# Kernel optimization log

Hardware: AMD Instinct MI355X
Metric: run time of the kernel (lower is better)

Reference implementation:

```python
import jax, jax.numpy as jnp
import numpy as np

N_NODES = 100000
N_EDGES = 3200000
IN_SIZE = 256
HID_SIZE = 256
OUT_SIZE = 64


def setup_inputs() -> dict:
    key = jax.random.key(0)
    ks = jax.random.split(key, 8)
    X = jax.random.normal(ks[0], (N_NODES, IN_SIZE), dtype=jnp.float32)
    edge_vals = jax.random.uniform(ks[1], (N_EDGES,), dtype=jnp.float32)
    # xavier-uniform-ish init for weights
    lim1 = float(np.sqrt(6.0 / (IN_SIZE + HID_SIZE)))
    W1 = jax.random.uniform(ks[2], (IN_SIZE, HID_SIZE), minval=-lim1, maxval=lim1, dtype=jnp.float32)
    b1 = jnp.zeros((HID_SIZE,), dtype=jnp.float32)
    lim2 = float(np.sqrt(6.0 / (HID_SIZE + OUT_SIZE)))
    W2 = jax.random.uniform(ks[3], (HID_SIZE, OUT_SIZE), minval=-lim2, maxval=lim2, dtype=jnp.float32)
    b2 = jnp.zeros((OUT_SIZE,), dtype=jnp.float32)
    row = jnp.sort(jax.random.randint(ks[4], (N_EDGES,), 0, N_NODES, dtype=jnp.int32))
    col = jax.random.randint(ks[5], (N_EDGES,), 0, N_NODES, dtype=jnp.int32)
    return {"X": X, "edge_vals": edge_vals, "W1": W1, "b1": b1,
            "W2": W2, "b2": b2, "row": row, "col": col}


def reference(X, edge_vals, W1, b1, W2, b2, row, col):
    """2-layer GCN (eval mode, dropout = identity).

    A is a sparse NxN matrix in COO form: A[row[e], col[e]] = edge_vals[e].
    Layer: relu(A @ (X @ W1) + b1); output: A @ (h @ W2) + b2.
    """
    n = X.shape[0]

    def spmm(dense):  # (A @ dense): gather columns, scale, segment-sum over rows
        gathered = edge_vals[:, None] * dense[col]        # [E, F]
        return jax.ops.segment_sum(gathered, row, num_segments=n)

    h = spmm(X @ W1) + b1          # [N, HID]
    h = jax.nn.relu(h)
    out = spmm(h @ W2) + b2        # [N, OUT]
    return out
```

## Files before the change

### kernel.cpp

```cpp
#include <hip/hip_runtime.h>


constexpr int IN_SIZE = 256;
constexpr int HID = 256;
constexpr int OUTF = 64;

typedef __bf16 bf16x8 __attribute__((ext_vector_type(8)));
typedef float f32x4 __attribute__((ext_vector_type(4)));

__device__ __forceinline__ ushort f2b(float f) {
    uint u = __float_as_uint(f);
    uint r = (u + 0x7fffu + ((u >> 16) & 1u)) >> 16;
    return (ushort)r;
}
__device__ __forceinline__ float b2f(ushort h) {
    return __uint_as_float(((uint)h) << 16);
}

__global__ void build_rowptr(const int* __restrict__ row, int* __restrict__ rp,
                             int n, int E) {
    int i = blockIdx.x * blockDim.x + threadIdx.x;
    if (i > n) return;
    int lo = 0, hi = E;
    while (lo < hi) {
        int mid = (lo + hi) >> 1;
        if (row[mid] < i) lo = mid + 1; else hi = mid;
    }
    rp[i] = lo;
}

__global__ void transpose_cast(const float* __restrict__ in, ushort* __restrict__ out,
                               int K, int N) {
    int n = blockIdx.x;
    int k = threadIdx.x;
    if (k < K) out[(size_t)n * K + k] = f2b(in[(size_t)k * N + n]);
}

__global__ __launch_bounds__(256, 2)
void gemm1_cast_n256(const float* __restrict__ A, const ushort* __restrict__ Bt,
                     ushort* __restrict__ C, int M) {
    constexpr int K = 256;
    __shared__ ushort As[128 * 40];
    __shared__ ushort Bs[256 * 40];
    const int tid = threadIdx.x;
    const int wave = tid >> 6, lane = tid & 63;
    const int quad = lane >> 4, l = lane & 15;
    const int wr = wave >> 1, wc = wave & 1;
    const int m0 = blockIdx.x * 128;

    const int ar = tid >> 1;
    const int ah = (tid & 1) * 16;
    const size_t aoff = (size_t)min(m0 + ar, M - 1) * K + ah;
    const int bn = tid >> 2;
    const int bkp = (tid & 3) * 8;

    f32x4 acc[4][8] = {};

    for (int k0 = 0; k0 < K; k0 += 32) {
        float4 a0 = *(const float4*)(A + aoff + k0);
        float4 a1 = *(const float4*)(A + aoff + k0 + 4);
        float4 a2 = *(const float4*)(A + aoff + k0 + 8);
        float4 a3 = *(const float4*)(A + aoff + k0 + 12);
        uint4 bv[4];
#pragma unroll
        for (int j = 0; j < 4; ++j)
            bv[j] = *(const uint4*)(Bt + (size_t)(bn + 64 * j) * K + k0 + bkp);
        uint4 pa0, pa1;
        pa0.x = (uint)f2b(a0.x) | ((uint)f2b(a0.y) << 16);
        pa0.y = (uint)f2b(a0.z) | ((uint)f2b(a0.w) << 16);
        pa0.z = (uint)f2b(a1.x) | ((uint)f2b(a1.y) << 16);
        pa0.w = (uint)f2b(a1.z) | ((uint)f2b(a1.w) << 16);
        pa1.x = (uint)f2b(a2.x) | ((uint)f2b(a2.y) << 16);
        pa1.y = (uint)f2b(a2.z) | ((uint)f2b(a2.w) << 16);
        pa1.z = (uint)f2b(a3.x) | ((uint)f2b(a3.y) << 16);
        pa1.w = (uint)f2b(a3.z) | ((uint)f2b(a3.w) << 16);
        __syncthreads();
        *(uint4*)&As[ar * 40 + ah] = pa0;
        *(uint4*)&As[ar * 40 + ah + 8] = pa1;
#pragma unroll
        for (int j = 0; j < 4; ++j)
            *(uint4*)&Bs[(bn + 64 * j) * 40 + bkp] = bv[j];
        __syncthreads();

        bf16x8 af[4], bfr[8];
        const ushort* ab = &As[(wr * 64 + l) * 40 + quad * 8];
#pragma unroll
        for (int mt = 0; mt < 4; ++mt)
            af[mt] = *(const bf16x8*)(ab + mt * 16 * 40);
        const ushort* bb = &Bs[(wc * 128 + l) * 40 + quad * 8];
#pragma unroll
        for (int nt = 0; nt < 8; ++nt)
            bfr[nt] = *(const bf16x8*)(bb + nt * 16 * 40);
#pragma unroll
        for (int mt = 0; mt < 4; ++mt)
#pragma unroll
            for (int nt = 0; nt < 8; ++nt)
                acc[mt][nt] = __builtin_amdgcn_mfma_f32_16x16x32_bf16(
                    af[mt], bfr[nt], acc[mt][nt], 0, 0, 0);
    }

#pragma unroll
    for (int mt = 0; mt < 4; ++mt)
#pragma unroll
        for (int nt = 0; nt < 8; ++nt)
#pragma unroll
            for (int reg = 0; reg < 4; ++reg) {
                int r = m0 + wr * 64 + mt * 16 + quad * 4 + reg;
                int c = wc * 128 + nt * 16 + l;
                if (r < M) C[(size_t)r * 256 + c] = f2b(acc[mt][nt][reg]);
            }
}

__global__ __launch_bounds__(256, 4)
void gemm_bf16(const ushort* __restrict__ A, const ushort* __restrict__ Bt,
               ushort* __restrict__ C, int M, int N, int K) {
    __shared__ ushort As[128 * 40];
    __shared__ ushort Bs[64 * 40];
    const int tid = threadIdx.x;
    const int wave = tid >> 6, lane = tid & 63;
    const int quad = lane >> 4, l = lane & 15;
    const int wr = wave >> 1, wc = wave & 1;
    const int m0 = blockIdx.x * 128, n0 = blockIdx.y * 64;

    const int crow = tid >> 2;
    const int cpart = (tid & 3) * 8;
    const size_t aoff0 = (size_t)min(m0 + crow, M - 1) * K + cpart;
    const size_t aoff1 = (size_t)min(m0 + crow + 64, M - 1) * K + cpart;
    const size_t boff  = (size_t)(n0 + crow) * K + cpart;

    f32x4 acc[4][2] = {};

    for (int k0 = 0; k0 < K; k0 += 32) {
        uint4 a0 = *(const uint4*)(A + aoff0 + k0);
        uint4 a1 = *(const uint4*)(A + aoff1 + k0);
        uint4 b0 = *(const uint4*)(Bt + boff + k0);
        __syncthreads();
        *(uint4*)&As[crow * 40 + cpart] = a0;
        *(uint4*)&As[(crow + 64) * 40 + cpart] = a1;
        *(uint4*)&Bs[crow * 40 + cpart] = b0;
        __syncthreads();

        bf16x8 af[4], bfr[2];
        const ushort* ab = &As[(wr * 64 + l) * 40 + quad * 8];
#pragma unroll
        for (int mt = 0; mt < 4; ++mt)
            af[mt] = *(const bf16x8*)(ab + mt * 16 * 40);
        const ushort* bb = &Bs[(wc * 32 + l) * 40 + quad * 8];
#pragma unroll
        for (int nt = 0; nt < 2; ++nt)
            bfr[nt] = *(const bf16x8*)(bb + nt * 16 * 40);
#pragma unroll
        for (int mt = 0; mt < 4; ++mt)
#pragma unroll
            for (int nt = 0; nt < 2; ++nt)
                acc[mt][nt] = __builtin_amdgcn_mfma_f32_16x16x32_bf16(
                    af[mt], bfr[nt], acc[mt][nt], 0, 0, 0);
    }

#pragma unroll
    for (int mt = 0; mt < 4; ++mt)
#pragma unroll
        for (int nt = 0; nt < 2; ++nt)
#pragma unroll
            for (int reg = 0; reg < 4; ++reg) {
                int r = m0 + wr * 64 + mt * 16 + quad * 4 + reg;
                int c = n0 + wc * 32 + nt * 16 + l;
                if (r < M) C[(size_t)r * N + c] = f2b(acc[mt][nt][reg]);
            }
}

__global__ __launch_bounds__(256)
void quant_rows_256(const ushort* __restrict__ Sb, char* __restrict__ Q,
                    float* __restrict__ scale, int n) {
    const int wave = threadIdx.x >> 6;
    const int lane = threadIdx.x & 63;
    const int node = blockIdx.x * 4 + wave;
    if (node >= n) return;
    ushort4 x = *(const ushort4*)(Sb + (size_t)node * 256 + lane * 4);
    float f0 = b2f(x.x), f1 = b2f(x.y), f2 = b2f(x.z), f3 = b2f(x.w);
    float am = fmaxf(fmaxf(fabsf(f0), fabsf(f1)), fmaxf(fabsf(f2), fabsf(f3)));
#pragma unroll
    for (int s = 32; s >= 1; s >>= 1) am = fmaxf(am, __shfl_xor(am, s));
    float inv = am > 0.f ? 127.f / am : 0.f;
    int q0 = (int)rintf(f0 * inv), q1 = (int)rintf(f1 * inv);
    int q2 = (int)rintf(f2 * inv), q3 = (int)rintf(f3 * inv);
    uint qp = ((uint)q0 & 0xff) | (((uint)q1 & 0xff) << 8) |
              (((uint)q2 & 0xff) << 16) | (((uint)q3 & 0xff) << 24);
    *(uint*)(Q + (size_t)node * 256 + lane * 4) = qp;
    if (lane == 0) scale[node] = am * (1.f / 127.f);
}

__global__ __launch_bounds__(256)
void quant_rows_64(const ushort* __restrict__ Sb, char* __restrict__ Q,
                   float* __restrict__ scale, int n) {
    const int wave = threadIdx.x >> 6;
    const int lane = threadIdx.x & 63;
    const int node = blockIdx.x * 4 + wave;
    if (node >= n) return;
    float f = b2f(Sb[(size_t)node * 64 + lane]);
    float am = fabsf(f);
#pragma unroll
    for (int s = 32; s >= 1; s >>= 1) am = fmaxf(am, __shfl_xor(am, s));
    float inv = am > 0.f ? 127.f / am : 0.f;
    Q[(size_t)node * 64 + lane] = (char)(int)rintf(f * inv);
    if (lane == 0) scale[node] = am * (1.f / 127.f);
}

__global__ __launch_bounds__(256)
void spmm1_q(const char* __restrict__ Q, const float* __restrict__ s1,
             const float* __restrict__ vals, const int* __restrict__ col,
             const int* __restrict__ rp, const float* __restrict__ bias,
             ushort* __restrict__ H, int n) {
    const int wave = threadIdx.x >> 6;
    const int lane = threadIdx.x & 63;
    const int node = blockIdx.x * 4 + wave;
    if (node >= n) return;
    const int e0 = rp[node], e1 = rp[node + 1];
    float a0 = 0.f, a1 = 0.f, a2 = 0.f, a3 = 0.f;
    int e = e0;
    for (; e + 7 < e1; e += 8) {
#pragma unroll
        for (int u = 0; u < 8; ++u) {
            int c = col[e + u];
            float f = vals[e + u] * s1[c];
            char4 q = *(const char4*)(Q + (size_t)c * 256 + lane * 4);
            a0 += f * (float)q.x;
            a1 += f * (float)q.y;
            a2 += f * (float)q.z;
            a3 += f * (float)q.w;
        }
    }
    for (; e < e1; ++e) {
        int c = col[e];
        float f = vals[e] * s1[c];
        char4 q = *(const char4*)(Q + (size_t)c * 256 + lane * 4);
        a0 += f * (float)q.x;
        a1 += f * (float)q.y;
        a2 += f * (float)q.z;
        a3 += f * (float)q.w;
    }
    float4 b = *(const float4*)(bias + lane * 4);
    ushort4 r;
    r.x = f2b(fmaxf(a0 + b.x, 0.f));
    r.y = f2b(fmaxf(a1 + b.y, 0.f));
    r.z = f2b(fmaxf(a2 + b.z, 0.f));
    r.w = f2b(fmaxf(a3 + b.w, 0.f));
    *(ushort4*)(H + (size_t)node * 256 + lane * 4) = r;
}

__global__ __launch_bounds__(256)
void spmm2_q(const char* __restrict__ Q, const float* __restrict__ s2,
             const float* __restrict__ vals, const int* __restrict__ col,
             const int* __restrict__ rp, const float* __restrict__ bias,
             float* __restrict__ O, int n) {
    const int wave = threadIdx.x >> 6;
    const int lane = threadIdx.x & 63;
    const int node = blockIdx.x * 4 + wave;
    if (node >= n) return;
    const int e0 = rp[node], e1 = rp[node + 1];
    float acc = 0.f;
    int e = e0;
    for (; e + 7 < e1; e += 8) {
#pragma unroll
        for (int u = 0; u < 8; ++u) {
            int c = col[e + u];
            float f = vals[e + u] * s2[c];
            acc += f * (float)Q[(size_t)c * 64 + lane];
        }
    }
    for (; e < e1; ++e) {
        int c = col[e];
        acc += vals[e] * s2[c] * (float)Q[(size_t)c * 64 + lane];
    }
    O[(size_t)node * 64 + lane] = acc + bias[lane];
}

static inline size_t alignup(size_t x) { return (x + 255) & ~(size_t)255; }

extern "C" void kernel_launch(void* const* d_in, const int* in_sizes, int n_in,
                              void* d_out, int out_size, void* d_ws, size_t ws_size,
                              hipStream_t stream) {
    const float* X  = (const float*)d_in[0];
    const float* ev = (const float*)d_in[1];
    const float* W1 = (const float*)d_in[2];
    const float* b1 = (const float*)d_in[3];
    const float* W2 = (const float*)d_in[4];
    const float* b2 = (const float*)d_in[5];
    const int*  row = (const int*)d_in[6];
    const int*  col = (const int*)d_in[7];
    float* out = (float*)d_out;

    const int n = in_sizes[0] / IN_SIZE;
    const int E = in_sizes[1];

    char* p = (char*)d_ws;
    ushort* C1  = (ushort*)p; p += alignup((size_t)n * HID * 2);
    char*   Q1  = (char*)p;   p += alignup((size_t)n * HID);
    float*  s1  = (float*)p;  p += alignup((size_t)n * 4);
    ushort* H   = (ushort*)p; p += alignup((size_t)n * HID * 2);
    ushort* hw2 = (ushort*)p; p += alignup((size_t)n * OUTF * 2);
    char*   Q2  = (char*)p;   p += alignup((size_t)n * OUTF);
    float*  s2  = (float*)p;  p += alignup((size_t)n * 4);
    ushort* W1T = (ushort*)p; p += alignup((size_t)IN_SIZE * HID * 2);
    ushort* W2T = (ushort*)p; p += alignup((size_t)HID * OUTF * 2);
    int*    rp  = (int*)p;

    build_rowptr<<<(n + 1 + 255) / 256, 256, 0, stream>>>(row, rp, n, E);
    transpose_cast<<<dim3(HID, 1), 256, 0, stream>>>(W1, W1T, IN_SIZE, HID);
    transpose_cast<<<dim3(OUTF, 1), 256, 0, stream>>>(W2, W2T, HID, OUTF);

    gemm1_cast_n256<<<(n + 127) / 128, 256, 0, stream>>>(X, W1T, C1, n);

    quant_rows_256<<<(n + 3) / 4, 256, 0, stream>>>(C1, Q1, s1, n);

    spmm1_q<<<(n + 3) / 4, 256, 0, stream>>>(Q1, s1, ev, col, rp, b1, H, n);

    dim3 g2((n + 127) / 128, OUTF / 64);
    gemm_bf16<<<g2, 256, 0, stream>>>(H, W2T, hw2, n, OUTF, HID);

    quant_rows_64<<<(n + 3) / 4, 256, 0, stream>>>(hw2, Q2, s2, n);

    spmm2_q<<<(n + 3) / 4, 256, 0, stream>>>(Q2, s2, ev, col, rp, b2, out, n);
}
```

Before: 525.2 us.

## Precompute packed edge (col, scaled weight) arrays and shrink GEMM1 tile

Adds a prep_edges kernel that folds the per-node quantization scale into each edge value and packs it with the column index as an int2. Both SpMM kernels then read that array instead of col, vals and a random s[c] gather. This removes a dependent random load per edge at the cost of an extra pass over the edges writing and reading E*8 bytes per layer. GEMM1 moves to 64-row tiles with one wave per 64-column slice, and the C1/H buffers are aliased to cut workspace footprint.

```diff
diff --git a/kernel.cpp b/kernel.cpp
--- a/kernel.cpp
+++ b/kernel.cpp
@@ -36,65 +36,64 @@
     if (k < K) out[(size_t)n * K + k] = f2b(in[(size_t)k * N + n]);
 }
 
-__global__ __launch_bounds__(256, 2)
-void gemm1_cast_n256(const float* __restrict__ A, const ushort* __restrict__ Bt,
-                     ushort* __restrict__ C, int M) {
+__global__ void prep_edges(const float* __restrict__ vals, const int* __restrict__ col,
+                           const float* __restrict__ s, int2* __restrict__ ew, int E) {
+    int e = blockIdx.x * 256 + threadIdx.x;
+    if (e >= E) return;
+    int c = col[e];
+    float w = vals[e] * s[c];
+    ew[e] = make_int2(c, __float_as_int(w));
+}
+
+__global__ __launch_bounds__(256)
+void gemm1_cast(const float* __restrict__ A, const ushort* __restrict__ Bt,
+                ushort* __restrict__ C, int M) {
     constexpr int K = 256;
-    __shared__ ushort As[128 * 40];
+    __shared__ ushort As[64 * 40];
     __shared__ ushort Bs[256 * 40];
     const int tid = threadIdx.x;
     const int wave = tid >> 6, lane = tid & 63;
     const int quad = lane >> 4, l = lane & 15;
-    const int wr = wave >> 1, wc = wave & 1;
-    const int m0 = blockIdx.x * 128;
-
-    const int ar = tid >> 1;
-    const int ah = (tid & 1) * 16;
-    const size_t aoff = (size_t)min(m0 + ar, M - 1) * K + ah;
+    const int m0 = blockIdx.x * 64;
+
+    const int ar = tid >> 2;
+    const int ak = (tid & 3) * 8;
+    const size_t aoff = (size_t)min(m0 + ar, M - 1) * K + ak;
     const int bn = tid >> 2;
     const int bkp = (tid & 3) * 8;
 
-    f32x4 acc[4][8] = {};
+    f32x4 acc[4][4] = {};
 
     for (int k0 = 0; k0 < K; k0 += 32) {
         float4 a0 = *(const float4*)(A + aoff + k0);
         float4 a1 = *(const float4*)(A + aoff + k0 + 4);
-        float4 a2 = *(const float4*)(A + aoff + k0 + 8);
-        float4 a3 = *(const float4*)(A + aoff + k0 + 12);
         uint4 bv[4];
 #pragma unroll
         for (int j = 0; j < 4; ++j)
             bv[j] = *(const uint4*)(Bt + (size_t)(bn + 64 * j) * K + k0 + bkp);
-        uint4 pa0, pa1;
-        pa0.x = (uint)f2b(a0.x) | ((uint)f2b(a0.y) << 16);
-        pa0.y = (uint)f2b(a0.z) | ((uint)f2b(a0.w) << 16);
-        pa0.z = (uint)f2b(a1.x) | ((uint)f2b(a1.y) << 16);
-        pa0.w = (uint)f2b(a1.z) | ((uint)f2b(a1.w) << 16);
-        pa1.x = (uint)f2b(a2.x) | ((uint)f2b(a2.y) << 16);
-        pa1.y = (uint)f2b(a2.z) | ((uint)f2b(a2.w) << 16);
-        pa1.z = (uint)f2b(a3.x) | ((uint)f2b(a3.y) << 16);
-        pa1.w = (uint)f2b(a3.z) | ((uint)f2b(a3.w) << 16);
+        uint4 pa;
+        pa.x = (uint)f2b(a0.x) | ((uint)f2b(a0.y) << 16);
+        pa.y = (uint)f2b(a0.z) | ((uint)f2b(a0.w) << 16);
+        pa.z = (uint)f2b(a1.x) | ((uint)f2b(a1.y) << 16);
+        pa.w = (uint)f2b(a1.z) | ((uint)f2b(a1.w) << 16);
         __syncthreads();
-        *(uint4*)&As[ar * 40 + ah] = pa0;
-        *(uint4*)&As[ar * 40 + ah + 8] = pa1;
+        *(uint4*)&As[ar * 40 + ak] = pa;
 #pragma unroll
         for (int j = 0; j < 4; ++j)
             *(uint4*)&Bs[(bn + 64 * j) * 40 + bkp] = bv[j];
         __syncthreads();
 
-        bf16x8 af[4], bfr[8];
-        const ushort* ab = &As[(wr * 64 + l) * 40 + quad * 8];
+        bf16x8 af[4], bfr[4];
 #pragma unroll
         for (int mt = 0; mt < 4; ++mt)
-            af[mt] = *(const bf16x8*)(ab + mt * 16 * 40);
-        const ushort* bb = &Bs[(wc * 128 + l) * 40 + quad * 8];
-#pragma unroll
-        for (int nt = 0; nt < 8; ++nt)
-            bfr[nt] = *(const bf16x8*)(bb + nt * 16 * 40);
+            af[mt] = *(const bf16x8*)&As[(mt * 16 + l) * 40 + quad * 8];
+#pragma unroll
+        for (int nt = 0; nt < 4; ++nt)
+            bfr[nt] = *(const bf16x8*)&Bs[(wave * 64 + nt * 16 + l) * 40 + quad * 8];
 #pragma unroll
         for (int mt = 0; mt < 4; ++mt)
 #pragma unroll
-            for (int nt = 0; nt < 8; ++nt)
+            for (int nt = 0; nt < 4; ++nt)
                 acc[mt][nt] = __builtin_amdgcn_mfma_f32_16x16x32_bf16(
                     af[mt], bfr[nt], acc[mt][nt], 0, 0, 0);
     }
@@ -102,11 +101,11 @@
 #pragma unroll
     for (int mt = 0; mt < 4; ++mt)
 #pragma unroll
-        for (int nt = 0; nt < 8; ++nt)
+        for (int nt = 0; nt < 4; ++nt)
 #pragma unroll
             for (int reg = 0; reg < 4; ++reg) {
-                int r = m0 + wr * 64 + mt * 16 + quad * 4 + reg;
-                int c = wc * 128 + nt * 16 + l;
+                int r = m0 + mt * 16 + quad * 4 + reg;
+                int c = wave * 64 + nt * 16 + l;
                 if (r < M) C[(size_t)r * 256 + c] = f2b(acc[mt][nt][reg]);
             }
 }
@@ -207,8 +206,7 @@
 }
 
 __global__ __launch_bounds__(256)
-void spmm1_q(const char* __restrict__ Q, const float* __restrict__ s1,
-             const float* __restrict__ vals, const int* __restrict__ col,
+void spmm1_q(const char* __restrict__ Q, const int2* __restrict__ ew,
              const int* __restrict__ rp, const float* __restrict__ bias,
              ushort* __restrict__ H, int n) {
     const int wave = threadIdx.x >> 6;
@@ -221,23 +219,23 @@
     for (; e + 7 < e1; e += 8) {
 #pragma unroll
         for (int u = 0; u < 8; ++u) {
-            int c = col[e + u];
-            float f = vals[e + u] * s1[c];
-            char4 q = *(const char4*)(Q + (size_t)c * 256 + lane * 4);
-            a0 += f * (float)q.x;
-            a1 += f * (float)q.y;
-            a2 += f * (float)q.z;
-            a3 += f * (float)q.w;
+            int2 m = ew[e + u];
+            float w = __int_as_float(m.y);
+            char4 q = *(const char4*)(Q + (size_t)m.x * 256 + lane * 4);
+            a0 += w * (float)q.x;
+            a1 += w * (float)q.y;
+            a2 += w * (float)q.z;
+            a3 += w * (float)q.w;
         }
     }
     for (; e < e1; ++e) {
-        int c = col[e];
-        float f = vals[e] * s1[c];
-        char4 q = *(const char4*)(Q + (size_t)c * 256 + lane * 4);
-        a0 += f * (float)q.x;
-        a1 += f * (float)q.y;
-        a2 += f * (float)q.z;
-        a3 += f * (float)q.w;
+        int2 m = ew[e];
+        float w = __int_as_float(m.y);
+        char4 q = *(const char4*)(Q + (size_t)m.x * 256 + lane * 4);
+        a0 += w * (float)q.x;
+        a1 += w * (float)q.y;
+        a2 += w * (float)q.z;
+        a3 += w * (float)q.w;
     }
     float4 b = *(const float4*)(bias + lane * 4);
     ushort4 r;
@@ -249,8 +247,7 @@
 }
 
 __global__ __launch_bounds__(256)
-void spmm2_q(const char* __restrict__ Q, const float* __restrict__ s2,
-             const float* __restrict__ vals, const int* __restrict__ col,
+void spmm2_q(const char* __restrict__ Q, const int2* __restrict__ ew,
              const int* __restrict__ rp, const float* __restrict__ bias,
              float* __restrict__ O, int n) {
     const int wave = threadIdx.x >> 6;
@@ -263,14 +260,13 @@
     for (; e + 7 < e1; e += 8) {
 #pragma unroll
         for (int u = 0; u < 8; ++u) {
-            int c = col[e + u];
-            float f = vals[e + u] * s2[c];
-            acc += f * (float)Q[(size_t)c * 64 + lane];
+            int2 m = ew[e + u];
+            acc += __int_as_float(m.y) * (float)Q[(size_t)m.x * 64 + lane];
         }
     }
     for (; e < e1; ++e) {
-        int c = col[e];
-        acc += vals[e] * s2[c] * (float)Q[(size_t)c * 64 + lane];
+        int2 m = ew[e];
+        acc += __int_as_float(m.y) * (float)Q[(size_t)m.x * 64 + lane];
     }
     O[(size_t)node * 64 + lane] = acc + bias[lane];
 }
@@ -294,31 +290,35 @@
     const int E = in_sizes[1];
 
     char* p = (char*)d_ws;
-    ushort* C1  = (ushort*)p; p += alignup((size_t)n * HID * 2);
-    char*   Q1  = (char*)p;   p += alignup((size_t)n * HID);
-    float*  s1  = (float*)p;  p += alignup((size_t)n * 4);
-    ushort* H   = (ushort*)p; p += alignup((size_t)n * HID * 2);
-    ushort* hw2 = (ushort*)p; p += alignup((size_t)n * OUTF * 2);
-    char*   Q2  = (char*)p;   p += alignup((size_t)n * OUTF);
-    float*  s2  = (float*)p;  p += alignup((size_t)n * 4);
-    ushort* W1T = (ushort*)p; p += alignup((size_t)IN_SIZE * HID * 2);
-    ushort* W2T = (ushort*)p; p += alignup((size_t)HID * OUTF * 2);
-    int*    rp  = (int*)p;
+    ushort* bufA = (ushort*)p; p += alignup((size_t)n * HID * 2);
+    char*   Q1   = (char*)p;   p += alignup((size_t)n * HID);
+    float*  s1   = (float*)p;  p += alignup((size_t)n * 4);
+    ushort* hw2  = (ushort*)p; p += alignup((size_t)n * OUTF * 2);
+    char*   Q2   = (char*)p;   p += alignup((size_t)n * OUTF);
+    float*  s2   = (float*)p;  p += alignup((size_t)n * 4);
+    ushort* W1T  = (ushort*)p; p += alignup((size_t)IN_SIZE * HID * 2);
+    ushort* W2T  = (ushort*)p; p += alignup((size_t)HID * OUTF * 2);
+    int*    rp   = (int*)p;    p += alignup((size_t)(n + 1) * 4);
+    int2*   ewb  = (int2*)p;   p += alignup((size_t)E * 8);
 
     build_rowptr<<<(n + 1 + 255) / 256, 256, 0, stream>>>(row, rp, n, E);
     transpose_cast<<<dim3(HID, 1), 256, 0, stream>>>(W1, W1T, IN_SIZE, HID);
     transpose_cast<<<dim3(OUTF, 1), 256, 0, stream>>>(W2, W2T, HID, OUTF);
 
-    gemm1_cast_n256<<<(n + 127) / 128, 256, 0, stream>>>(X, W1T, C1, n);
-
-    quant_rows_256<<<(n + 3) / 4, 256, 0, stream>>>(C1, Q1, s1, n);
-
-    spmm1_q<<<(n + 3) / 4, 256, 0, stream>>>(Q1, s1, ev, col, rp, b1, H, n);
+    gemm1_cast<<<(n + 63) / 64, 256, 0, stream>>>(X, W1T, bufA, n);
+
+    quant_rows_256<<<(n + 3) / 4, 256, 0, stream>>>(bufA, Q1, s1, n);
+
+    prep_edges<<<(E + 255) / 256, 256, 0, stream>>>(ev, col, s1, ewb, E);
+
+    spmm1_q<<<(n + 3) / 4, 256, 0, stream>>>(Q1, ewb, rp, b1, bufA, n);
 
     dim3 g2((n + 127) / 128, OUTF / 64);
-    gemm_bf16<<<g2, 256, 0, stream>>>(H, W2T, hw2, n, OUTF, HID);
+    gemm_bf16<<<g2, 256, 0, stream>>>(bufA, W2T, hw2, n, OUTF, HID);
 
     quant_rows_64<<<(n + 3) / 4, 256, 0, stream>>>(hw2, Q2, s2, n);
 
-    spmm2_q<<<(n + 3) / 4, 256, 0, stream>>>(Q2, s2, ev, col, rp, b2, out, n);
-}
+    prep_edges<<<(E + 255) / 256, 256, 0, stream>>>(ev, col, s2, ewb, E);
+
+    spmm2_q<<<(n + 3) / 4, 256, 0, stream>>>(Q2, ewb, rp, b2, out, n);
+}
```

Result: slower. 570.8 us (+8.7%).
